# Performance work log

Measured on AMD Instinct MI355X. Metric: run time of the kernel, lower is better.

## Reference

```python
import jax, jax.numpy as jnp
import numpy as np
from functools import partial

HIDDEN = 512
INTER = 2048
N_EXPERTS = 8
TOP_K = 2
BATCH, SEQ = 2, 2048


def setup_inputs() -> dict:
    key = jax.random.key(0)
    k_x, k_r, k_u, k_d = jax.random.split(key, 4)
    x = jax.random.normal(k_x, (BATCH, SEQ, HIDDEN), dtype=jnp.float32)
    # router: nn.Linear(hidden, n_experts, bias=False); store as (H, E) so logits = x @ w_router
    w_router = jax.random.normal(k_r, (HIDDEN, N_EXPERTS), dtype=jnp.float32) / np.sqrt(HIDDEN)
    # per-expert FFN weights, stored pre-transposed for x @ W
    w_up = jax.random.normal(k_u, (N_EXPERTS, HIDDEN, INTER), dtype=jnp.float32) / np.sqrt(HIDDEN)
    w_down = jax.random.normal(k_d, (N_EXPERTS, INTER, HIDDEN), dtype=jnp.float32) / np.sqrt(INTER)
    return {"x": x, "w_router": w_router, "w_up": w_up, "w_down": w_down}


def _moe_forward(x, w_router, w_up, w_down):
    B, S, H = x.shape
    T = B * S
    xf = x.reshape(T, H)
    logits = xf @ w_router                      # (T, E)
    top_vals, top_idx = jax.lax.top_k(logits, TOP_K)
    rw = jax.nn.softmax(top_vals, axis=-1)      # (T, K) routing weights
    E = w_up.shape[0]
    # combine weight per (token, expert): sum_k rw[t,k] * [sel[t,k]==e]
    cw = jnp.zeros((T, E), dtype=x.dtype).at[
        jnp.arange(T)[:, None], top_idx
    ].add(rw)                                   # (T, E)

    def expert_step(acc, operand):
        wu, wd, we = operand                    # (H,I), (I,H), (T,)
        h = jax.nn.gelu(xf @ wu, approximate=False)  # exact erf GELU (torch nn.GELU default)
        y = h @ wd                              # (T, H)
        return acc + we[:, None] * y, None

    acc0 = jnp.zeros((T, H), dtype=x.dtype)
    acc, _ = jax.lax.scan(expert_step, acc0, (w_up, w_down, cw.T))
    output = acc.reshape(B, S, H)

    # aux load-balance loss
    probs = jax.nn.softmax(logits, axis=-1)
    expert_usage = probs.mean(axis=0)           # (E,)
    load_balance_loss = jnp.sum((expert_usage - 1.0 / E) ** 2)
    return output, load_balance_loss, expert_usage


def reference(x, w_router, w_up, w_down):
    return _moe_forward(x, w_router, w_up, w_down)
```

## Files before the change

### kernel.cpp

```cpp
#include <hip/hip_runtime.h>
#include <hip/hip_bf16.h>
#include <math.h>

#define T_TOKENS 4096
#define HID 512
#define INTER 2048
#define NEXP 8

typedef __bf16 bf16x8 __attribute__((ext_vector_type(8)));
typedef __bf16 bf16x4 __attribute__((ext_vector_type(4)));
typedef float f32x4 __attribute__((ext_vector_type(4)));

#define GLD16(g, l) __builtin_amdgcn_global_load_lds( \
    (const __attribute__((address_space(1))) void*)(g), \
    (__attribute__((address_space(3))) void*)(l), 16, 0, 0)

__device__ __forceinline__ void transpose_tile(const float* __restrict__ in,
                                               __bf16* __restrict__ out,
                                               int R, int C, int r0, int c0,
                                               __bf16 (*tile)[68]) {
  int tid = threadIdx.x;
  int rr = tid >> 4;
  int cc = (tid & 15) * 4;
#pragma unroll
  for (int j = 0; j < 4; ++j) {
    int row = j * 16 + rr;
    float4 v = *(const float4*)(in + (size_t)(r0 + row) * C + c0 + cc);
    tile[row][cc + 0] = (__bf16)v.x;
    tile[row][cc + 1] = (__bf16)v.y;
    tile[row][cc + 2] = (__bf16)v.z;
    tile[row][cc + 3] = (__bf16)v.w;
  }
  __syncthreads();
#pragma unroll
  for (int j = 0; j < 4; ++j) {
    int orow = j * 16 + rr;
    bf16x4 o;
    o[0] = tile[cc + 0][orow];
    o[1] = tile[cc + 1][orow];
    o[2] = tile[cc + 2][orow];
    o[3] = tile[cc + 3][orow];
    *(bf16x4*)(out + (size_t)(c0 + orow) * R + r0 + cc) = o;
  }
}

__global__ void prep_kernel(const float* __restrict__ x, const float* __restrict__ wrt,
                            int* __restrict__ topi, float* __restrict__ topw,
                            int* __restrict__ cntpart, float* __restrict__ usagepart,
                            const float* __restrict__ wu, __bf16* __restrict__ wuT,
                            const float* __restrict__ wd, __bf16* __restrict__ wdT) {
  __shared__ float wsm[8 * 512];
  __shared__ float us[8];
  __shared__ int cs[8];
  __shared__ __bf16 tile[64][68];
  int bid = blockIdx.x;
  int tid = threadIdx.x;

  if (bid >= 3072) {
    int b = bid - 3072;
    int e = b >> 8;
    int c0 = (b & 7) * 64;
    int r0 = ((b >> 3) & 31) * 64;
    transpose_tile(wd + (size_t)e * INTER * HID, wdT + (size_t)e * INTER * HID,
                   INTER, HID, r0, c0, tile);
    return;
  }
  if (bid >= 1024) {
    int b = bid - 1024;
    int e = b >> 8;
    int c0 = (b & 31) * 64;
    int r0 = ((b >> 5) & 7) * 64;
    transpose_tile(wu + (size_t)e * HID * INTER, wuT + (size_t)e * HID * INTER,
                   HID, INTER, r0, c0, tile);
    return;
  }

  if (tid < 8) { us[tid] = 0.f; cs[tid] = 0; }
  for (int i = tid; i < 8 * 512; i += 256) {
    int e = i >> 9, h = i & 511;
    wsm[i] = wrt[h * 8 + e];
  }
  __syncthreads();
  int lane = tid & 63;
  int t = bid * 4 + (tid >> 6);
  const float* xt = x + (size_t)t * HID;
  float a[8];
#pragma unroll
  for (int e = 0; e < 8; ++e) a[e] = 0.f;
#pragma unroll
  for (int j = 0; j < 8; ++j) {
    float xv = xt[lane + j * 64];
#pragma unroll
    for (int e = 0; e < 8; ++e) a[e] += xv * wsm[e * 512 + lane + j * 64];
  }
#pragma unroll
  for (int off = 32; off > 0; off >>= 1) {
#pragma unroll
    for (int e = 0; e < 8; ++e) a[e] += __shfl_xor(a[e], off);
  }
  if (lane == 0) {
    float m = a[0];
#pragma unroll
    for (int e = 1; e < 8; ++e) m = fmaxf(m, a[e]);
    float p[8], s = 0.f;
#pragma unroll
    for (int e = 0; e < 8; ++e) { p[e] = expf(a[e] - m); s += p[e]; }
    float inv = 1.f / s;
#pragma unroll
    for (int e = 0; e < 8; ++e) atomicAdd(&us[e], p[e] * inv);
    int i0 = 0; float v0 = a[0];
#pragma unroll
    for (int e = 1; e < 8; ++e) if (a[e] > v0) { v0 = a[e]; i0 = e; }
    int i1 = -1; float v1 = -3.4e38f;
#pragma unroll
    for (int e = 0; e < 8; ++e) if (e != i0 && a[e] > v1) { v1 = a[e]; i1 = e; }
    float e1 = expf(v1 - v0);
    float w0 = 1.f / (1.f + e1);
    float w1 = e1 * w0;
    topi[t * 2] = i0; topi[t * 2 + 1] = i1;
    topw[t * 2] = w0; topw[t * 2 + 1] = w1;
    atomicAdd(&cs[i0], 1); atomicAdd(&cs[i1], 1);
  }
  __syncthreads();
  if (tid < 8) {
    cntpart[bid * 8 + tid] = cs[tid];
    usagepart[bid * 8 + tid] = us[tid];
  }
}

__global__ void finalize_kernel(const int* __restrict__ cntpart, const float* __restrict__ usagepart,
                                int* __restrict__ cnt, int* __restrict__ off,
                                float* __restrict__ tail) {
  __shared__ int ci[256];
  __shared__ float uf[256];
  int tid = threadIdx.x;
  int e = tid >> 5, c = tid & 31;
  int s = 0; float u = 0.f;
  for (int b = c; b < 1024; b += 32) {
    s += cntpart[b * 8 + e];
    u += usagepart[b * 8 + e];
  }
  ci[tid] = s; uf[tid] = u;
  __syncthreads();
  for (int st = 16; st > 0; st >>= 1) {
    if (c < st) { ci[tid] += ci[tid + st]; uf[tid] += uf[tid + st]; }
    __syncthreads();
  }
  if (tid == 0) {
    int o = 0;
    float loss = 0.f;
    for (int e2 = 0; e2 < 8; ++e2) {
      int ce = ci[e2 * 32];
      cnt[e2] = ce;
      off[e2] = o;
      o += (ce + 127) & ~127;
      float uu = uf[e2 * 32] * (1.0f / 4096.0f);
      tail[1 + e2] = uu;
      float d = uu - 0.125f;
      loss += d * d;
    }
    tail[0] = loss;
  }
}

__global__ void slotassign_kernel(const int* __restrict__ topi, const float* __restrict__ topw,
                                  const int* __restrict__ off, int* __restrict__ cnt2pad,
                                  int* __restrict__ stok, float* __restrict__ sw,
                                  int* __restrict__ slotof) {
  __shared__ int wavehist[16][8];
  __shared__ int blockbase[8];
  int tid = threadIdx.x, lane = tid & 63, wv = tid >> 6;
  int p = blockIdx.x * 1024 + tid;
  int e = topi[p];
  float w = topw[p];
  unsigned long long mymask = 0;
#pragma unroll
  for (int e2 = 0; e2 < 8; ++e2) {
    unsigned long long m = __ballot(e == e2);
    if (lane == 0) wavehist[wv][e2] = __popcll(m);
    if (e2 == e) mymask = m;
  }
  __syncthreads();
  if (tid < 8) {
    int s = 0;
#pragma unroll
    for (int w2 = 0; w2 < 16; ++w2) s += wavehist[w2][tid];
    blockbase[tid] = atomicAdd(&cnt2pad[tid * 16], s);
  }
  __syncthreads();
  int rank = 0;
  for (int w2 = 0; w2 < wv; ++w2) rank += wavehist[w2][e];
  rank += __popcll(mymask & ((1ull << lane) - 1ull));
  int slot = off[e] + blockbase[e] + rank;
  stok[slot] = p >> 1;
  sw[slot] = w;
  slotof[p] = slot;
}

__global__ void gather_kernel(const float* __restrict__ x, const int* __restrict__ slotof,
                              __bf16* __restrict__ Xg) {
  int tid = threadIdx.x, lane = tid & 63;
  int p = blockIdx.x * 4 + (tid >> 6);
  int slot = slotof[p];
  int t = p >> 1;
  const float4* xs = (const float4*)(x + (size_t)t * HID);
  float4 v0 = xs[lane * 2], v1 = xs[lane * 2 + 1];
  bf16x8 o;
  o[0] = (__bf16)v0.x; o[1] = (__bf16)v0.y; o[2] = (__bf16)v0.z; o[3] = (__bf16)v0.w;
  o[4] = (__bf16)v1.x; o[5] = (__bf16)v1.y; o[6] = (__bf16)v1.z; o[7] = (__bf16)v1.w;
  *(bf16x8*)(Xg + (size_t)slot * HID + lane * 8) = o;
}

template <int EPI>
__launch_bounds__(256, 6)
__global__ void gemm64(const __bf16* __restrict__ A, const __bf16* __restrict__ Ball,
                       int lda, int ldb, long sB,
                       __bf16* __restrict__ Hout, int ldh,
                       float* __restrict__ Out,
                       const int* __restrict__ stok, const float* __restrict__ sw,
                       const int* __restrict__ offp, const int* __restrict__ cntp) {
  int bid = blockIdx.x;
  int e = bid & 7;
  int r = bid >> 3;
  int mt, n0, nk;
  if (EPI == 0) {
    n0 = (r & 31) * 64;
    mt = r >> 5;
    nk = 8;
  } else {
    n0 = (r & 7) * 64;
    mt = r >> 3;
    nk = 32;
  }
  int cnte = cntp[e];
  if (mt * 64 >= cnte) return;
  int offe = offp[e];
  int m0 = offe + mt * 64;
  const __bf16* B = Ball + (size_t)e * sB;

  __shared__ char smem[16384];
  char* As = smem;
  char* Bs = smem + 8192;

  int tid = threadIdx.x;
  int lane = tid & 63;
  int wid = tid >> 6;
  int wr = wid >> 1, wc = wid & 1;

  f32x4 acc[2][2];
#pragma unroll
  for (int i = 0; i < 2; ++i)
#pragma unroll
    for (int j = 0; j < 2; ++j) acc[i][j] = (f32x4){0.f, 0.f, 0.f, 0.f};

  for (int it = 0; it < nk; ++it) {
    int k0 = it * 64;
#pragma unroll
    for (int q2 = 0; q2 < 2; ++q2) {
      int L = q2 * 4096 + tid * 16;
      int row = L >> 7;
      int kb = L & 127;
      int kbs = kb ^ ((row & 7) << 4);
      GLD16((const char*)(A + (size_t)(m0 + row) * lda + k0) + kbs, As + L);
      GLD16((const char*)(B + (size_t)(n0 + row) * (size_t)ldb + k0) + kbs, Bs + L);
    }
    __syncthreads();
#pragma unroll
    for (int ks = 0; ks < 2; ++ks) {
      bf16x8 av[2], bv[2];
      int kb = ks * 64 + ((lane >> 4) << 4);
#pragma unroll
      for (int i = 0; i < 2; ++i) {
        int rowA = wr * 32 + i * 16 + (lane & 15);
        av[i] = *(const bf16x8*)(As + rowA * 128 + (kb ^ ((rowA & 7) << 4)));
        int rowB = wc * 32 + i * 16 + (lane & 15);
        bv[i] = *(const bf16x8*)(Bs + rowB * 128 + (kb ^ ((rowB & 7) << 4)));
      }
#pragma unroll
      for (int i = 0; i < 2; ++i)
#pragma unroll
        for (int j = 0; j < 2; ++j)
          acc[i][j] = __builtin_amdgcn_mfma_f32_16x16x32_bf16(av[i], bv[j], acc[i][j], 0, 0, 0);
    }
    __syncthreads();
  }

  int lim = offe + cnte;
  if (EPI == 0) {
#pragma unroll
    for (int i = 0; i < 2; ++i) {
#pragma unroll
      for (int r2 = 0; r2 < 4; ++r2) {
        int slot = m0 + wr * 32 + i * 16 + ((lane >> 4) << 2) + r2;
        if (slot < lim) {
          __bf16* hp = Hout + (size_t)slot * ldh + n0 + wc * 32 + (lane & 15);
#pragma unroll
          for (int j = 0; j < 2; ++j) {
            float v = acc[i][j][r2];
            float g = 0.5f * v * (1.0f + erff(v * 0.70710678118654752f));
            hp[j * 16] = (__bf16)g;
          }
        }
      }
    }
  } else {
#pragma unroll
    for (int i = 0; i < 2; ++i) {
#pragma unroll
      for (int r2 = 0; r2 < 4; ++r2) {
        int slot = m0 + wr * 32 + i * 16 + ((lane >> 4) << 2) + r2;
        if (slot < lim) {
          int t = stok[slot];
          float w = sw[slot];
          float* op = Out + (size_t)t * HID + n0 + wc * 32 + (lane & 15);
#pragma unroll
          for (int j = 0; j < 2; ++j) atomicAdd(op + j * 16, w * acc[i][j][r2]);
        }
      }
    }
  }
}

extern "C" void kernel_launch(void* const* d_in, const int* in_sizes, int n_in,
                              void* d_out, int out_size, void* d_ws, size_t ws_size,
                              hipStream_t stream) {
  const float* x   = (const float*)d_in[0];
  const float* wrt = (const float*)d_in[1];
  const float* wu  = (const float*)d_in[2];
  const float* wd  = (const float*)d_in[3];
  float* out = (float*)d_out;
  char* ws = (char*)d_ws;

  const size_t XG_OFF   = 0;
  const size_t H_OFF    = XG_OFF  + (size_t)9216 * 512 * 2;
  const size_t WUT_OFF  = H_OFF   + (size_t)9216 * 2048 * 2;
  const size_t WDT_OFF  = WUT_OFF + (size_t)8 * 512 * 2048 * 2;
  const size_t TOK_OFF  = WDT_OFF + (size_t)8 * 512 * 2048 * 2;
  const size_t SW_OFF   = TOK_OFF  + (size_t)9216 * 4;
  const size_t TOPI_OFF = SW_OFF   + (size_t)9216 * 4;
  const size_t TOPW_OFF = TOPI_OFF + (size_t)8192 * 4;
  const size_t SLOT_OFF = TOPW_OFF + (size_t)8192 * 4;
  const size_t CPART_OFF = SLOT_OFF + (size_t)8192 * 4;
  const size_t UPART_OFF = CPART_OFF + (size_t)8192 * 4;
  const size_t CTRL_OFF  = UPART_OFF + (size_t)8192 * 4;

  __bf16* Xg   = (__bf16*)(ws + XG_OFF);
  __bf16* H    = (__bf16*)(ws + H_OFF);
  __bf16* wuT  = (__bf16*)(ws + WUT_OFF);
  __bf16* wdT  = (__bf16*)(ws + WDT_OFF);
  int*    stok = (int*)(ws + TOK_OFF);
  float*  sw   = (float*)(ws + SW_OFF);
  int*    topi = (int*)(ws + TOPI_OFF);
  float*  topw = (float*)(ws + TOPW_OFF);
  int*    slotof = (int*)(ws + SLOT_OFF);
  int*    cntpart = (int*)(ws + CPART_OFF);
  float*  usagepart = (float*)(ws + UPART_OFF);
  int*    cnt  = (int*)(ws + CTRL_OFF);
  int*    off  = (int*)(ws + CTRL_OFF + 64);
  int*    cnt2pad = (int*)(ws + CTRL_OFF + 128);

  hipMemsetAsync(ws + CTRL_OFF, 0, 1024, stream);
  hipMemsetAsync(d_out, 0, (size_t)T_TOKENS * HID * 4, stream);

  prep_kernel<<<5120, 256, 0, stream>>>(x, wrt, topi, topw, cntpart, usagepart,
                                        wu, wuT, wd, wdT);
  finalize_kernel<<<1, 256, 0, stream>>>(cntpart, usagepart, cnt, off,
                                         out + (size_t)T_TOKENS * HID);
  slotassign_kernel<<<8, 1024, 0, stream>>>(topi, topw, off, cnt2pad, stok, sw, slotof);
  gather_kernel<<<2048, 256, 0, stream>>>(x, slotof, Xg);

  gemm64<0><<<6144, 256, 0, stream>>>(
      Xg, wuT, HID, HID, (long)INTER * HID, H, INTER,
      nullptr, nullptr, nullptr, off, cnt);
  gemm64<1><<<1536, 256, 0, stream>>>(
      H, wdT, INTER, INTER, (long)INTER * HID, nullptr, 0,
      out, stok, sw, off, cnt);
}
```

Before: 123.4 us.

## Keep up-projection weight tile resident in LDS across multiple row tiles

The up-projection GEMM now loads a 64x512 weight slice for one expert into 64KB of shared memory once per block. Each block then loops over up to 12 row tiles of gathered tokens, streaming only the activation tiles, so weight reloads from global memory are removed. The grid drops from 6144 to 512 blocks and occupancy falls to 2 blocks per CU because of the larger LDS footprint. This risks fewer waves in flight to hide latency and load imbalance when expert token counts are uneven. The down-projection GEMM is split into its own kernel and is otherwise unchanged.

```diff
diff --git a/kernel.cpp b/kernel.cpp
--- a/kernel.cpp
+++ b/kernel.cpp
@@ -211,89 +211,96 @@
   *(bf16x8*)(Xg + (size_t)slot * HID + lane * 8) = o;
 }
 
-template <int EPI>
-__launch_bounds__(256, 6)
-__global__ void gemm64(const __bf16* __restrict__ A, const __bf16* __restrict__ Ball,
-                       int lda, int ldb, long sB,
-                       __bf16* __restrict__ Hout, int ldh,
-                       float* __restrict__ Out,
-                       const int* __restrict__ stok, const float* __restrict__ sw,
-                       const int* __restrict__ offp, const int* __restrict__ cntp) {
+__launch_bounds__(256, 2)
+__global__ void gemm_up_bres(const __bf16* __restrict__ A, const __bf16* __restrict__ Ball,
+                             __bf16* __restrict__ Hout,
+                             const int* __restrict__ offp, const int* __restrict__ cntp) {
   int bid = blockIdx.x;
   int e = bid & 7;
   int r = bid >> 3;
-  int mt, n0, nk;
-  if (EPI == 0) {
-    n0 = (r & 31) * 64;
-    mt = r >> 5;
-    nk = 8;
-  } else {
-    n0 = (r & 7) * 64;
-    mt = r >> 3;
-    nk = 32;
-  }
+  int nt = r & 31;
+  int mh = r >> 5;
+  int n0 = nt * 64;
   int cnte = cntp[e];
-  if (mt * 64 >= cnte) return;
+  int mts = mh * 12;
+  if (mts * 64 >= cnte) return;
   int offe = offp[e];
-  int m0 = offe + mt * 64;
-  const __bf16* B = Ball + (size_t)e * sB;
-
-  __shared__ char smem[16384];
-  char* As = smem;
-  char* Bs = smem + 8192;
+  const __bf16* B = Ball + (size_t)e * INTER * HID;
+
+  __shared__ char smem[73728];
+  char* Bres = smem;
+  char* As = smem + 65536;
 
   int tid = threadIdx.x;
   int lane = tid & 63;
   int wid = tid >> 6;
   int wr = wid >> 1, wc = wid & 1;
 
-  f32x4 acc[2][2];
-#pragma unroll
-  for (int i = 0; i < 2; ++i)
-#pragma unroll
-    for (int j = 0; j < 2; ++j) acc[i][j] = (f32x4){0.f, 0.f, 0.f, 0.f};
-
-  for (int it = 0; it < nk; ++it) {
-    int k0 = it * 64;
-#pragma unroll
-    for (int q2 = 0; q2 < 2; ++q2) {
-      int L = q2 * 4096 + tid * 16;
+#pragma unroll
+  for (int c = 0; c < 8; ++c) {
+#pragma unroll
+    for (int q = 0; q < 2; ++q) {
+      int L = q * 4096 + tid * 16;
       int row = L >> 7;
       int kb = L & 127;
       int kbs = kb ^ ((row & 7) << 4);
-      GLD16((const char*)(A + (size_t)(m0 + row) * lda + k0) + kbs, As + L);
-      GLD16((const char*)(B + (size_t)(n0 + row) * (size_t)ldb + k0) + kbs, Bs + L);
-    }
-    __syncthreads();
-#pragma unroll
-    for (int ks = 0; ks < 2; ++ks) {
-      bf16x8 av[2], bv[2];
-      int kb = ks * 64 + ((lane >> 4) << 4);
-#pragma unroll
-      for (int i = 0; i < 2; ++i) {
-        int rowA = wr * 32 + i * 16 + (lane & 15);
-        av[i] = *(const bf16x8*)(As + rowA * 128 + (kb ^ ((rowA & 7) << 4)));
-        int rowB = wc * 32 + i * 16 + (lane & 15);
-        bv[i] = *(const bf16x8*)(Bs + rowB * 128 + (kb ^ ((rowB & 7) << 4)));
+      GLD16((const char*)(B + (size_t)(n0 + row) * HID + c * 64) + kbs,
+            Bres + c * 8192 + L);
+    }
+  }
+  __syncthreads();
+
+  int lim = offe + cnte;
+  for (int m = 0; m < 12; ++m) {
+    int mt = mts + m;
+    if (mt * 64 >= cnte) break;
+    int m0 = offe + mt * 64;
+
+    f32x4 acc[2][2];
+#pragma unroll
+    for (int i = 0; i < 2; ++i)
+#pragma unroll
+      for (int j = 0; j < 2; ++j) acc[i][j] = (f32x4){0.f, 0.f, 0.f, 0.f};
+
+    for (int it = 0; it < 8; ++it) {
+      int k0 = it * 64;
+#pragma unroll
+      for (int q2 = 0; q2 < 2; ++q2) {
+        int L = q2 * 4096 + tid * 16;
+        int row = L >> 7;
+        int kb = L & 127;
+        int kbs = kb ^ ((row & 7) << 4);
+        GLD16((const char*)(A + (size_t)(m0 + row) * HID + k0) + kbs, As + L);
       }
-#pragma unroll
-      for (int i = 0; i < 2; ++i)
-#pragma unroll
-        for (int j = 0; j < 2; ++j)
-          acc[i][j] = __builtin_amdgcn_mfma_f32_16x16x32_bf16(av[i], bv[j], acc[i][j], 0, 0, 0);
-    }
-    __syncthreads();
-  }
-
-  int lim = offe + cnte;
-  if (EPI == 0) {
+      __syncthreads();
+      const char* Bc = Bres + it * 8192;
+#pragma unroll
+      for (int ks = 0; ks < 2; ++ks) {
+        bf16x8 av[2], bv[2];
+        int kb = ks * 64 + ((lane >> 4) << 4);
+#pragma unroll
+        for (int i = 0; i < 2; ++i) {
+          int rowA = wr * 32 + i * 16 + (lane & 15);
+          av[i] = *(const bf16x8*)(As + rowA * 128 + (kb ^ ((rowA & 7) << 4)));
+          int rowB = wc * 32 + i * 16 + (lane & 15);
+          bv[i] = *(const bf16x8*)(Bc + rowB * 128 + (kb ^ ((rowB & 7) << 4)));
+        }
+#pragma unroll
+        for (int i = 0; i < 2; ++i)
+#pragma unroll
+          for (int j = 0; j < 2; ++j)
+            acc[i][j] = __builtin_amdgcn_mfma_f32_16x16x32_bf16(av[i], bv[j], acc[i][j], 0, 0, 0);
+      }
+      __syncthreads();
+    }
+
 #pragma unroll
     for (int i = 0; i < 2; ++i) {
 #pragma unroll
       for (int r2 = 0; r2 < 4; ++r2) {
         int slot = m0 + wr * 32 + i * 16 + ((lane >> 4) << 2) + r2;
         if (slot < lim) {
-          __bf16* hp = Hout + (size_t)slot * ldh + n0 + wc * 32 + (lane & 15);
+          __bf16* hp = Hout + (size_t)slot * INTER + n0 + wc * 32 + (lane & 15);
 #pragma unroll
           for (int j = 0; j < 2; ++j) {
             float v = acc[i][j][r2];
@@ -303,19 +310,84 @@
         }
       }
     }
-  } else {
-#pragma unroll
-    for (int i = 0; i < 2; ++i) {
-#pragma unroll
-      for (int r2 = 0; r2 < 4; ++r2) {
-        int slot = m0 + wr * 32 + i * 16 + ((lane >> 4) << 2) + r2;
-        if (slot < lim) {
-          int t = stok[slot];
-          float w = sw[slot];
-          float* op = Out + (size_t)t * HID + n0 + wc * 32 + (lane & 15);
-#pragma unroll
-          for (int j = 0; j < 2; ++j) atomicAdd(op + j * 16, w * acc[i][j][r2]);
-        }
+  }
+}
+
+__launch_bounds__(256, 6)
+__global__ void gemm_down(const __bf16* __restrict__ A, const __bf16* __restrict__ Ball,
+                          float* __restrict__ Out,
+                          const int* __restrict__ stok, const float* __restrict__ sw,
+                          const int* __restrict__ offp, const int* __restrict__ cntp) {
+  int bid = blockIdx.x;
+  int e = bid & 7;
+  int r = bid >> 3;
+  int n0 = (r & 7) * 64;
+  int mt = r >> 3;
+  int cnte = cntp[e];
+  if (mt * 64 >= cnte) return;
+  int offe = offp[e];
+  int m0 = offe + mt * 64;
+  const __bf16* B = Ball + (size_t)e * INTER * HID;
+
+  __shared__ char smem[16384];
+  char* As = smem;
+  char* Bs = smem + 8192;
+
+  int tid = threadIdx.x;
+  int lane = tid & 63;
+  int wid = tid >> 6;
+  int wr = wid >> 1, wc = wid & 1;
+
+  f32x4 acc[2][2];
+#pragma unroll
+  for (int i = 0; i < 2; ++i)
+#pragma unroll
+    for (int j = 0; j < 2; ++j) acc[i][j] = (f32x4){0.f, 0.f, 0.f, 0.f};
+
+  for (int it = 0; it < 32; ++it) {
+    int k0 = it * 64;
+#pragma unroll
+    for (int q2 = 0; q2 < 2; ++q2) {
+      int L = q2 * 4096 + tid * 16;
+      int row = L >> 7;
+      int kb = L & 127;
+      int kbs = kb ^ ((row & 7) << 4);
+      GLD16((const char*)(A + (size_t)(m0 + row) * INTER + k0) + kbs, As + L);
+      GLD16((const char*)(B + (size_t)(n0 + row) * INTER + k0) + kbs, Bs + L);
+    }
+    __syncthreads();
+#pragma unroll
+    for (int ks = 0; ks < 2; ++ks) {
+      bf16x8 av[2], bv[2];
+      int kb = ks * 64 + ((lane >> 4) << 4);
+#pragma unroll
+      for (int i = 0; i < 2; ++i) {
+        int rowA = wr * 32 + i * 16 + (lane & 15);
+        av[i] = *(const bf16x8*)(As + rowA * 128 + (kb ^ ((rowA & 7) << 4)));
+        int rowB = wc * 32 + i * 16 + (lane & 15);
+        bv[i] = *(const bf16x8*)(Bs + rowB * 128 + (kb ^ ((rowB & 7) << 4)));
+      }
+#pragma unroll
+      for (int i = 0; i < 2; ++i)
+#pragma unroll
+        for (int j = 0; j < 2; ++j)
+          acc[i][j] = __builtin_amdgcn_mfma_f32_16x16x32_bf16(av[i], bv[j], acc[i][j], 0, 0, 0);
+    }
+    __syncthreads();
+  }
+
+  int lim = offe + cnte;
+#pragma unroll
+  for (int i = 0; i < 2; ++i) {
+#pragma unroll
+    for (int r2 = 0; r2 < 4; ++r2) {
+      int slot = m0 + wr * 32 + i * 16 + ((lane >> 4) << 2) + r2;
+      if (slot < lim) {
+        int t = stok[slot];
+        float w = sw[slot];
+        float* op = Out + (size_t)t * HID + n0 + wc * 32 + (lane & 15);
+#pragma unroll
+        for (int j = 0; j < 2; ++j) atomicAdd(op + j * 16, w * acc[i][j][r2]);
       }
     }
   }
@@ -369,10 +441,6 @@
   slotassign_kernel<<<8, 1024, 0, stream>>>(topi, topw, off, cnt2pad, stok, sw, slotof);
   gather_kernel<<<2048, 256, 0, stream>>>(x, slotof, Xg);
 
-  gemm64<0><<<6144, 256, 0, stream>>>(
-      Xg, wuT, HID, HID, (long)INTER * HID, H, INTER,
-      nullptr, nullptr, nullptr, off, cnt);
-  gemm64<1><<<1536, 256, 0, stream>>>(
-      H, wdT, INTER, INTER, (long)INTER * HID, nullptr, 0,
-      out, stok, sw, off, cnt);
-}
+  gemm_up_bres<<<512, 256, 0, stream>>>(Xg, wuT, H, off, cnt);
+  gemm_down<<<1536, 256, 0, stream>>>(H, wdT, out, stok, sw, off, cnt);
+}
```

After: 161.9 us. 31.2% more time.
